# Kernel tuning notes

Measured on AMD Instinct MI355X. Metric: run time of the kernel, lower is better.

The kernel has to match this reference:

```python
import jax, jax.numpy as jnp
import numpy as np

WEIGHT_GROUP = 128  # in-channel group size for scales (module default)


def setup_inputs() -> dict:
    key = jax.random.key(0)
    k1, k2, k3, k4, k5 = jax.random.split(key, 5)
    B, IN, OUT = 16, 8192, 8192
    nG = IN // WEIGHT_GROUP  # 64 scale groups along in_features
    x = jax.random.normal(k1, (B, IN), dtype=jnp.float32)
    # 'weight' stores the already-quantized low-bit float values (small magnitudes)
    weight = jax.random.normal(k2, (OUT, IN), dtype=jnp.float32)
    # per-(row, group) positive scales
    scale_buf = jax.random.uniform(k3, (OUT, nG), dtype=jnp.float32, minval=0.01, maxval=1.0)
    bias = jax.random.normal(k4, (1, OUT), dtype=jnp.float32)
    # per-[64, group]-block mantissa-format ids in {0,1,2}; selects the dequant
    # format on hardware but is a constant lookup (no float math) in the reference
    types = jax.random.randint(k5, (OUT // 64, nG), 0, 3, dtype=jnp.int32)
    return {"x": x, "weight": weight, "scale_buf": scale_buf, "bias": bias, "types": types}


def reference(x, weight, scale_buf, bias, types):
    O, I = weight.shape
    nG = scale_buf.shape[1]
    G = I // nG
    # group-wise dequant: w_deq[o, g*G + j] = weight[o, g*G + j] * scale_buf[o, g]
    w_deq = (weight.reshape(O, nG, G) * scale_buf[:, :, None]).reshape(O, I)
    # y = x @ W_deq^T + bias   [B, O]
    return jnp.einsum("bi,oi->bo", x, w_deq) + bias
```

## Files before the change

### kernel.cpp

```cpp
#include <hip/hip_runtime.h>
#include <hip/hip_bf16.h>

#define IN_F 8192
#define OUT_F 8192
#define NB 16
#define NG 64
#define KSPLIT 8
#define KRANGE (IN_F / KSPLIT)
#define NSTEP (KRANGE / 32)
#define PF 8

typedef __attribute__((ext_vector_type(8))) short bf16x8;
typedef __attribute__((ext_vector_type(4))) float f32x4;

static __device__ __forceinline__ unsigned bfpack2(float a, float b) {
    unsigned ua = __float_as_uint(a) + 0x8000u;
    unsigned ub = __float_as_uint(b) + 0x8000u;
    return __builtin_amdgcn_perm(ub, ua, 0x07060302u);
}

__global__ __launch_bounds__(256)
void init_out_kernel(const float* __restrict__ bias, float* __restrict__ out) {
    const int i = blockIdx.x * 256 + threadIdx.x;
    out[i] = bias[i & (OUT_F - 1)];
}

__global__ __launch_bounds__(256, 4)
void axcore_mfma_kernel(const float* __restrict__ x,
                        const float* __restrict__ w,
                        const float* __restrict__ scale,
                        float* __restrict__ out) {
    __shared__ __align__(16) unsigned short xswz[NSTEP * 64 * 8];

    const int t    = threadIdx.x;
    const int lane = t & 63;
    const int k0   = blockIdx.y * KRANGE;
    const int o0   = blockIdx.x * 64 + (t >> 6) * 16;

#pragma unroll
    for (int p = 0; p < 16; ++p) {
        const int idx = p * 256 + t;
        const int m   = idx >> 8;
        const int k4  = (idx & 255) * 4;
        const float4 v = *(const float4*)&x[m * IN_F + k0 + k4];
        const int tt = k4 >> 5;
        const int ln = m + 16 * ((k4 & 31) >> 3);
        const int jj = k4 & 7;
        uint2 sv;
        sv.x = bfpack2(v.x, v.y);
        sv.y = bfpack2(v.z, v.w);
        *(uint2*)&xswz[(tt * 64 + ln) * 8 + jj] = sv;
    }
    __syncthreads();

    const int nrow = o0 + (lane & 15);
    const int koct = (lane >> 4) * 8;
    const float* wrow = &w[(size_t)nrow * IN_F + k0 + koct];

    const float4 sA = *(const float4*)&scale[nrow * NG + (k0 >> 7)];
    const float4 sB = *(const float4*)&scale[nrow * NG + (k0 >> 7) + 4];
    const float sg[8] = {sA.x, sA.y, sA.z, sA.w, sB.x, sB.y, sB.z, sB.w};

    float4 wbuf0[PF], wbuf1[PF];
#pragma unroll
    for (int i = 0; i < PF; ++i) {
        wbuf0[i] = *(const float4*)&wrow[i * 32];
        wbuf1[i] = *(const float4*)&wrow[i * 32 + 4];
    }

    f32x4 acc = {0.f, 0.f, 0.f, 0.f};

#pragma unroll
    for (int ts = 0; ts < NSTEP; ++ts) {
        const float4 w0 = wbuf0[ts % PF];
        const float4 w1 = wbuf1[ts % PF];
        if (ts + PF < NSTEP) {
            wbuf0[ts % PF] = *(const float4*)&wrow[(ts + PF) * 32];
            wbuf1[ts % PF] = *(const float4*)&wrow[(ts + PF) * 32 + 4];
        }
        const float s = sg[ts / 4];

        bf16x8 bfrag;
        unsigned* bu = (unsigned*)&bfrag;
        bu[0] = bfpack2(w0.x * s, w0.y * s);
        bu[1] = bfpack2(w0.z * s, w0.w * s);
        bu[2] = bfpack2(w1.x * s, w1.y * s);
        bu[3] = bfpack2(w1.z * s, w1.w * s);

        const bf16x8 afrag = *(const bf16x8*)&xswz[(ts * 64 + lane) * 8];

        acc = __builtin_amdgcn_mfma_f32_16x16x32_bf16(afrag, bfrag, acc, 0, 0, 0);
    }

#pragma unroll
    for (int r = 0; r < 4; ++r) {
        const int b = (lane >> 4) * 4 + r;
        atomicAdd(&out[b * OUT_F + nrow], acc[r]);
    }
}

extern "C" void kernel_launch(void* const* d_in, const int* in_sizes, int n_in,
                              void* d_out, int out_size, void* d_ws, size_t ws_size,
                              hipStream_t stream) {
    const float* x    = (const float*)d_in[0];
    const float* w    = (const float*)d_in[1];
    const float* sc   = (const float*)d_in[2];
    const float* bias = (const float*)d_in[3];
    float* out = (float*)d_out;

    hipLaunchKernelGGL(init_out_kernel, dim3(NB * OUT_F / 256), dim3(256),
                       0, stream, bias, out);
    hipLaunchKernelGGL(axcore_mfma_kernel, dim3(OUT_F / 64, KSPLIT), dim3(256),
                       0, stream, x, w, sc, out);
}
```

Before: 395.8 us.

## Stage dequantized weights through LDS with coalesced row loads and double the K split

Each wave now loads full weight rows with coalesced float4 accesses, dequantizes them to bf16 and writes them to a padded LDS tile. MFMA B fragments are then read from LDS instead of per-lane strided global loads. KSPLIT is doubled to 16 so there are more blocks and a smaller per-block K range, at the cost of twice as many output atomics. The register prefetch ring is removed and a sync is added per chunk, so loads are no longer overlapped with MFMA within a block and latency hiding depends on occupancy.

Result: faster. 376.6 us (-4.8%).

```diff
diff --git a/kernel.cpp b/kernel.cpp
--- a/kernel.cpp
+++ b/kernel.cpp
@@ -5,10 +5,12 @@
 #define OUT_F 8192
 #define NB 16
 #define NG 64
-#define KSPLIT 8
+#define KSPLIT 16
 #define KRANGE (IN_F / KSPLIT)
+#define BK 256
+#define NCHUNK (KRANGE / BK)
 #define NSTEP (KRANGE / 32)
-#define PF 8
+#define WSTRIDE 264
 
 typedef __attribute__((ext_vector_type(8))) short bf16x8;
 typedef __attribute__((ext_vector_type(4))) float f32x4;
@@ -25,23 +27,26 @@
     out[i] = bias[i & (OUT_F - 1)];
 }
 
-__global__ __launch_bounds__(256, 4)
+__global__ __launch_bounds__(256, 3)
 void axcore_mfma_kernel(const float* __restrict__ x,
                         const float* __restrict__ w,
                         const float* __restrict__ scale,
                         float* __restrict__ out) {
     __shared__ __align__(16) unsigned short xswz[NSTEP * 64 * 8];
+    __shared__ __align__(16) unsigned short wlds[64 * WSTRIDE];
 
     const int t    = threadIdx.x;
+    const int wv   = t >> 6;
     const int lane = t & 63;
     const int k0   = blockIdx.y * KRANGE;
-    const int o0   = blockIdx.x * 64 + (t >> 6) * 16;
+    const int ob   = blockIdx.x * 64;
+    const int o0   = ob + wv * 16;
 
 #pragma unroll
-    for (int p = 0; p < 16; ++p) {
+    for (int p = 0; p < 8; ++p) {
         const int idx = p * 256 + t;
-        const int m   = idx >> 8;
-        const int k4  = (idx & 255) * 4;
+        const int m   = idx >> 7;
+        const int k4  = (idx & 127) * 4;
         const float4 v = *(const float4*)&x[m * IN_F + k0 + k4];
         const int tt = k4 >> 5;
         const int ln = m + 16 * ((k4 & 31) >> 3);
@@ -51,45 +56,37 @@
         sv.y = bfpack2(v.z, v.w);
         *(uint2*)&xswz[(tt * 64 + ln) * 8 + jj] = sv;
     }
-    __syncthreads();
-
-    const int nrow = o0 + (lane & 15);
-    const int koct = (lane >> 4) * 8;
-    const float* wrow = &w[(size_t)nrow * IN_F + k0 + koct];
-
-    const float4 sA = *(const float4*)&scale[nrow * NG + (k0 >> 7)];
-    const float4 sB = *(const float4*)&scale[nrow * NG + (k0 >> 7) + 4];
-    const float sg[8] = {sA.x, sA.y, sA.z, sA.w, sB.x, sB.y, sB.z, sB.w};
-
-    float4 wbuf0[PF], wbuf1[PF];
-#pragma unroll
-    for (int i = 0; i < PF; ++i) {
-        wbuf0[i] = *(const float4*)&wrow[i * 32];
-        wbuf1[i] = *(const float4*)&wrow[i * 32 + 4];
-    }
 
     f32x4 acc = {0.f, 0.f, 0.f, 0.f};
+    const int nrow = o0 + (lane & 15);
 
 #pragma unroll
-    for (int ts = 0; ts < NSTEP; ++ts) {
-        const float4 w0 = wbuf0[ts % PF];
-        const float4 w1 = wbuf1[ts % PF];
-        if (ts + PF < NSTEP) {
-            wbuf0[ts % PF] = *(const float4*)&wrow[(ts + PF) * 32];
-            wbuf1[ts % PF] = *(const float4*)&wrow[(ts + PF) * 32 + 4];
+    for (int c = 0; c < NCHUNK; ++c) {
+        if (c > 0) __syncthreads();
+
+        const int kcg = k0 + c * BK;
+        const int gb  = kcg >> 7;
+#pragma unroll
+        for (int i = 0; i < 16; ++i) {
+            const int rl  = wv * 16 + i;
+            const int row = ob + rl;
+            const float4 v = *(const float4*)&w[(size_t)row * IN_F + kcg + 4 * lane];
+            const float s = scale[row * NG + gb + (lane >> 5)];
+            uint2 pk;
+            pk.x = bfpack2(v.x * s, v.y * s);
+            pk.y = bfpack2(v.z * s, v.w * s);
+            *(uint2*)&wlds[rl * WSTRIDE + lane * 4] = pk;
         }
-        const float s = sg[ts / 4];
+        __syncthreads();
 
-        bf16x8 bfrag;
-        unsigned* bu = (unsigned*)&bfrag;
-        bu[0] = bfpack2(w0.x * s, w0.y * s);
-        bu[1] = bfpack2(w0.z * s, w0.w * s);
-        bu[2] = bfpack2(w1.x * s, w1.y * s);
-        bu[3] = bfpack2(w1.z * s, w1.w * s);
-
-        const bf16x8 afrag = *(const bf16x8*)&xswz[(ts * 64 + lane) * 8];
-
-        acc = __builtin_amdgcn_mfma_f32_16x16x32_bf16(afrag, bfrag, acc, 0, 0, 0);
+#pragma unroll
+        for (int tl = 0; tl < BK / 32; ++tl) {
+            const int ts = c * (BK / 32) + tl;
+            const bf16x8 afrag = *(const bf16x8*)&xswz[(ts * 64 + lane) * 8];
+            const bf16x8 bfrag = *(const bf16x8*)
+                &wlds[(wv * 16 + (lane & 15)) * WSTRIDE + tl * 32 + (lane >> 4) * 8];
+            acc = __builtin_amdgcn_mfma_f32_16x16x32_bf16(afrag, bfrag, acc, 0, 0, 0);
+        }
     }
 
 #pragma unroll
```
